# Optimization experiments

Measured on AMD Instinct MI355X. Metric: run time of the kernel, lower is better.

Reference implementation:

```python
import jax, jax.numpy as jnp
import numpy as np

N = 100000
E = 1600000
IN_CH = 32
HID = 64
HEADS = 2
NUM_CLASSES = 12
NEG_SLOPE = 0.2


def gat_conv(x, src, dst, W, a_src, a_dst, bias, concat):
    """PyG-style GATConv (self-loops already appended to src/dst).
    x: [N, F_in], W: [F_in, H*C], a_src/a_dst: [H, C], bias: [H*C] or [C]."""
    n = x.shape[0]
    h = (x @ W).reshape(n, HEADS, -1)                    # [N, H, C]
    al_s = jnp.einsum('nhc,hc->nh', h, a_src)            # [N, H]
    al_d = jnp.einsum('nhc,hc->nh', h, a_dst)            # [N, H]
    e = jax.nn.leaky_relu(al_s[src] + al_d[dst], NEG_SLOPE)  # [Etot, H]
    # segment softmax over destination neighborhoods
    e_max = jax.ops.segment_max(e, dst, num_segments=n)      # [N, H]
    ex = jnp.exp(e - e_max[dst])                              # [Etot, H]
    denom = jax.ops.segment_sum(ex, dst, num_segments=n)     # [N, H]
    alpha = ex / denom[dst]                                   # [Etot, H]
    msg = h[src] * alpha[:, :, None]                          # [Etot, H, C]
    out = jax.ops.segment_sum(msg, dst, num_segments=n)      # [N, H, C]
    if concat:
        out = out.reshape(n, -1)
    else:
        out = out.mean(axis=1)
    return out + bias


def prelu(x, a):
    return jnp.where(x >= 0, x, a * x)


def setup_inputs() -> dict:
    key = jax.random.key(0)
    ks = jax.random.split(key, 16)
    HC = HEADS * HID
    d = {
        'x': jax.random.normal(ks[0], (N, IN_CH), jnp.float32),
        'edge_index': jax.random.randint(ks[1], (2, E), 0, N, jnp.int32),
        'W1': jax.random.normal(ks[2], (IN_CH, HC), jnp.float32) * 0.1,
        'a1s': jax.random.normal(ks[3], (HEADS, HID), jnp.float32) * 0.1,
        'a1d': jax.random.normal(ks[4], (HEADS, HID), jnp.float32) * 0.1,
        'b1': jnp.zeros((HC,), jnp.float32),
        'W2': jax.random.normal(ks[5], (HC, HC), jnp.float32) * 0.1,
        'a2s': jax.random.normal(ks[6], (HEADS, HID), jnp.float32) * 0.1,
        'a2d': jax.random.normal(ks[7], (HEADS, HID), jnp.float32) * 0.1,
        'b2': jnp.zeros((HC,), jnp.float32),
        'W3': jax.random.normal(ks[8], (HC, HC), jnp.float32) * 0.1,
        'a3s': jax.random.normal(ks[9], (HEADS, HID), jnp.float32) * 0.1,
        'a3d': jax.random.normal(ks[10], (HEADS, HID), jnp.float32) * 0.1,
        'b3': jnp.zeros((HID,), jnp.float32),
        'prelu_a': jnp.float32(0.25),
        'Wc': jax.random.normal(ks[11], (HID, NUM_CLASSES), jnp.float32) * 0.1,
        'bc': jnp.zeros((NUM_CLASSES,), jnp.float32),
    }
    return d


def reference(x, edge_index, W1, a1s, a1d, b1, W2, a2s, a2d, b2,
              W3, a3s, a3d, b3, prelu_a, Wc, bc):
    loops = jnp.arange(N, dtype=edge_index.dtype)
    src = jnp.concatenate([edge_index[0], loops])
    dst = jnp.concatenate([edge_index[1], loops])
    h = gat_conv(x, src, dst, W1, a1s, a1d, b1, concat=True)
    h = prelu(h, prelu_a)
    h = gat_conv(h, src, dst, W2, a2s, a2d, b2, concat=True)
    h = prelu(h, prelu_a)
    h = gat_conv(h, src, dst, W3, a3s, a3d, b3, concat=False)
    h = prelu(h, prelu_a)
    return h @ Wc + bc
```

## Files before the change

### kernel.cpp

```cpp
#include <hip/hip_runtime.h>
#include <stdint.h>

#define NN 100000
#define NE 1600000
#define ET (NE + NN)
#define HC 128
#define HID 64
#define NCLS 12
#define BSZ 512
#define NBK ((NN + BSZ - 1) / BSZ)
#define CHUNK 8192
#define NPB ((ET + CHUNK - 1) / CHUNK)

typedef _Float16 f16;
typedef _Float16 f16x2 __attribute__((ext_vector_type(2)));
typedef _Float16 f16x4 __attribute__((ext_vector_type(4)));
typedef _Float16 f16x8 __attribute__((ext_vector_type(8)));
typedef float f32x4 __attribute__((ext_vector_type(4)));

__global__ void k_init(int* bucketTotal) {
    int i = threadIdx.x;
    if (i < NBK) bucketTotal[i] = 0;
}

__global__ __launch_bounds__(256) void k_hist(const int* __restrict__ ei, int* __restrict__ bucketTotal) {
    __shared__ int h[NBK];
    int tid = threadIdx.x;
    for (int b = tid; b < NBK; b += 256) h[b] = 0;
    __syncthreads();
    long base = (long)blockIdx.x * CHUNK;
#pragma unroll
    for (int k = 0; k < CHUNK / 256; k++) {
        long i = base + k * 256 + tid;
        if (i < ET) {
            int d = (i < NE) ? ei[NE + i] : (int)(i - NE);
            atomicAdd(&h[d >> 9], 1);
        }
    }
    __syncthreads();
    for (int b = tid; b < NBK; b += 256)
        if (h[b]) atomicAdd(&bucketTotal[b], h[b]);
}

__global__ __launch_bounds__(256) void k_bscan(const int* __restrict__ bucketTotal,
                                               int* __restrict__ bucketStart,
                                               int* __restrict__ bucketFill,
                                               int* __restrict__ rp) {
    __shared__ int s[256];
    int tid = threadIdx.x;
    int v = (tid < NBK) ? bucketTotal[tid] : 0;
    s[tid] = v;
    __syncthreads();
    for (int o = 1; o < 256; o <<= 1) {
        int t = (tid >= o) ? s[tid - o] : 0;
        __syncthreads();
        s[tid] += t;
        __syncthreads();
    }
    if (tid < NBK) {
        int excl = s[tid] - v;
        bucketStart[tid] = excl;
        bucketFill[tid] = excl;
    }
    if (tid == 0) { bucketStart[NBK] = ET; rp[NN] = ET; }
}

__global__ __launch_bounds__(256) void k_part(const int* __restrict__ ei,
                                              int* __restrict__ bucketFill,
                                              uint32_t* __restrict__ ebuf) {
    __shared__ int h[NBK];
    __shared__ int base[NBK];
    int tid = threadIdx.x;
    for (int b = tid; b < NBK; b += 256) h[b] = 0;
    __syncthreads();
    long cbase = (long)blockIdx.x * CHUNK;
#pragma unroll
    for (int k = 0; k < CHUNK / 256; k++) {
        long i = cbase + k * 256 + tid;
        if (i < ET) {
            int d = (i < NE) ? ei[NE + i] : (int)(i - NE);
            atomicAdd(&h[d >> 9], 1);
        }
    }
    __syncthreads();
    for (int b = tid; b < NBK; b += 256)
        base[b] = h[b] ? atomicAdd(&bucketFill[b], h[b]) : 0;
    __syncthreads();
    for (int b = tid; b < NBK; b += 256) h[b] = 0;
    __syncthreads();
#pragma unroll
    for (int k = 0; k < CHUNK / 256; k++) {
        long i = cbase + k * 256 + tid;
        if (i < ET) {
            int s, d;
            if (i < NE) { s = ei[i]; d = ei[NE + i]; } else { s = d = (int)(i - NE); }
            int bk = d >> 9;
            int off = atomicAdd(&h[bk], 1);
            ebuf[base[bk] + off] = (uint32_t)s | ((uint32_t)(d & 511) << 17);
        }
    }
}

__global__ __launch_bounds__(512) void k_build(const uint32_t* __restrict__ ebuf,
                                               const int* __restrict__ bucketStart,
                                               int* __restrict__ rp, int* __restrict__ colx) {
    __shared__ int cnt[BSZ];
    __shared__ int fill[BSZ];
    int b = blockIdx.x, tid = threadIdx.x;
    int e0 = bucketStart[b], e1 = bucketStart[b + 1], m = e1 - e0;
    cnt[tid] = 0;
    __syncthreads();
    for (int k = tid; k < m; k += 512) atomicAdd(&cnt[ebuf[e0 + k] >> 17], 1);
    __syncthreads();
    int v = cnt[tid];
    __syncthreads();
    cnt[tid] = v;
    __syncthreads();
    for (int o = 1; o < 512; o <<= 1) {
        int t = (tid >= o) ? cnt[tid - o] : 0;
        __syncthreads();
        cnt[tid] += t;
        __syncthreads();
    }
    int excl = cnt[tid] - v;
    int node = b * BSZ + tid;
    if (node < NN) rp[node] = e0 + excl;
    fill[tid] = e0 + excl;
    __syncthreads();
    for (int k = tid; k < m; k += 512) {
        uint32_t e = ebuf[e0 + k];
        int pos = atomicAdd(&fill[e >> 17], 1);
        colx[pos] = (int)(e & 0x1FFFF);
    }
}

__global__ void k_wt(const float* __restrict__ W2, const float* __restrict__ W3,
                     f16* __restrict__ wout) {
    const float* W = blockIdx.x ? W3 : W2;
    f16* hi = wout + (size_t)blockIdx.x * 2 * 2048 * 8;
    f16* lo = hi + 2048 * 8;
    for (int s = threadIdx.x; s < 2048; s += 256) {
        int kk = s >> 9, nt = (s >> 6) & 7, l = s & 63;
        int n = nt * 16 + (l & 15), k0 = kk * 32 + (l >> 4) * 8;
        f16x8 vh, vl;
#pragma unroll
        for (int j = 0; j < 8; j++) {
            float v = W[(long)(k0 + j) * HC + n];
            f16 h = (f16)v;
            vh[j] = h;
            vl[j] = (f16)(v - (float)h);
        }
        *(f16x8*)(hi + (size_t)s * 8) = vh;
        *(f16x8*)(lo + (size_t)s * 8) = vl;
    }
}

__global__ __launch_bounds__(256) void k_att1(const float* __restrict__ x,
                                              const float* __restrict__ W1,
                                              const float* __restrict__ a1s,
                                              const float* __restrict__ a1d,
                                              f16* __restrict__ x16,
                                              float* __restrict__ als, float* __restrict__ ald) {
    __shared__ float sIn[128 * 33];
    __shared__ float spv[128];
    int t = threadIdx.x;
    long n0 = (long)blockIdx.x * 128;
    if (t < 128) {
        int sd = t >> 6, h = (t >> 5) & 1, f = t & 31;
        const float* a = sd ? a1d : a1s;
        float acc = 0.f;
        for (int c = 0; c < 64; c++) acc = fmaf(W1[f * HC + h * 64 + c], a[h * 64 + c], acc);
        spv[t] = acc;
    }
    for (int c = t; c < 128 * 8; c += 256) {
        int row = c >> 3, col = (c & 7) * 4;
        long gn = n0 + row;
        if (gn < NN) {
            float4 v = *(const float4*)(x + gn * 32 + col);
            float* dst = &sIn[row * 33 + col];
            dst[0] = v.x; dst[1] = v.y; dst[2] = v.z; dst[3] = v.w;
            f16x4 o;
            o[0] = (f16)v.x; o[1] = (f16)v.y; o[2] = (f16)v.z; o[3] = (f16)v.w;
            *(f16x4*)(x16 + gn * 32 + col) = o;
        }
    }
    __syncthreads();
    int n = t >> 1, h = t & 1;
    long gn = n0 + n;
    if (gn >= NN) return;
    const float* row = &sIn[n * 33];
    const float* as_ = &spv[h * 32];
    const float* ad_ = &spv[64 + h * 32];
    float s_ = 0.f, d_ = 0.f;
#pragma unroll
    for (int f = 0; f < 32; f++) {
        float v = row[f];
        s_ = fmaf(v, as_[f], s_);
        d_ = fmaf(v, ad_[f], d_);
    }
    als[2 * gn + h] = s_;
    ald[2 * gn + h] = d_;
}

__global__ __launch_bounds__(256) void k_aggx(const int* __restrict__ rp, const int* __restrict__ colx,
                                              const f16* __restrict__ x16,
                                              const float* __restrict__ als, const float* __restrict__ ald,
                                              float* __restrict__ xbar) {
    int wid = blockIdx.x * 4 + (threadIdx.x >> 6);
    int lane = threadIdx.x & 63;
    int g = lane >> 4, li = lane & 15;
    int start = rp[wid], end = rp[wid + 1];
    float2 adv = *(const float2*)(ald + 2 * wid);
    float a00 = 0.f, a01 = 0.f, a10 = 0.f, a11 = 0.f, ws0 = 0.f, ws1 = 0.f;
#pragma unroll 4
    for (int j0 = start; j0 < end; j0 += 4) {
        int j = j0 + g;
        int jc = j < end ? j : end - 1;
        int s = colx[jc];
        float2 asv = *(const float2*)(als + 2 * s);
        float e0 = asv.x + adv.x, e1 = asv.y + adv.y;
        e0 = fmaxf(e0, 0.2f * e0);
        e1 = fmaxf(e1, 0.2f * e1);
        float w0 = __expf(e0), w1 = __expf(e1);
        if (j >= end) { w0 = 0.f; w1 = 0.f; }
        ws0 += w0; ws1 += w1;
        f16x2 xv = *(const f16x2*)(x16 + (long)s * 32 + li * 2);
        float f0 = (float)xv[0], f1 = (float)xv[1];
        a00 = fmaf(w0, f0, a00); a01 = fmaf(w0, f1, a01);
        a10 = fmaf(w1, f0, a10); a11 = fmaf(w1, f1, a11);
    }
#pragma unroll
    for (int o = 16; o <= 32; o <<= 1) {
        ws0 += __shfl_xor(ws0, o); ws1 += __shfl_xor(ws1, o);
        a00 += __shfl_xor(a00, o); a01 += __shfl_xor(a01, o);
        a10 += __shfl_xor(a10, o); a11 += __shfl_xor(a11, o);
    }
    if (g == 0) {
        float inv = 1.0f / ws0;
        *(float2*)(xbar + (long)wid * 64 + li * 2) = make_float2(a00 * inv, a01 * inv);
    } else if (g == 1) {
        float inv = 1.0f / ws1;
        *(float2*)(xbar + (long)wid * 64 + 32 + li * 2) = make_float2(a10 * inv, a11 * inv);
    }
}

__global__ __launch_bounds__(256) void k_post1(const float* __restrict__ xb,
                                               const float* __restrict__ W1,
                                               const float* __restrict__ b1,
                                               const float* __restrict__ pap,
                                               f16* __restrict__ outp) {
    __shared__ __align__(16) float sIn[64 * 64];
    __shared__ __align__(16) float sW[32 * HC];
    __shared__ float sB[HC];
    int tid = threadIdx.x;
    long n0 = (long)blockIdx.x * 64;
    for (int c = tid; c < 64 * 16; c += 256) {
        int row = c >> 4, col = (c & 15) * 4;
        long gn = n0 + row;
        float4 v = make_float4(0.f, 0.f, 0.f, 0.f);
        if (gn < NN) v = *(const float4*)(xb + gn * 64 + col);
        *(float4*)(sIn + row * 64 + col) = v;
    }
    for (int c = tid; c < 32 * HC / 4; c += 256) ((float4*)sW)[c] = ((const float4*)W1)[c];
    if (tid < HC) sB[tid] = b1[tid];
    __syncthreads();
    int cg = tid & 31, ng = tid >> 5, head = cg >> 4;
    float4 acc[8];
#pragma unroll
    for (int i = 0; i < 8; i++) acc[i] = make_float4(0.f, 0.f, 0.f, 0.f);
    for (int k = 0; k < 32; k++) {
        float4 w = *(const float4*)(sW + k * HC + cg * 4);
#pragma unroll
        for (int i = 0; i < 8; i++) {
            float a = sIn[(ng * 8 + i) * 64 + head * 32 + k];
            acc[i].x = fmaf(a, w.x, acc[i].x);
            acc[i].y = fmaf(a, w.y, acc[i].y);
            acc[i].z = fmaf(a, w.z, acc[i].z);
            acc[i].w = fmaf(a, w.w, acc[i].w);
        }
    }
    float pa = pap[0];
    float4 b = *(const float4*)(sB + cg * 4);
#pragma unroll
    for (int i = 0; i < 8; i++) {
        long n = n0 + ng * 8 + i;
        if (n < NN) {
            float o0 = acc[i].x + b.x, o1 = acc[i].y + b.y;
            float o2 = acc[i].z + b.z, o3 = acc[i].w + b.w;
            o0 = o0 >= 0.f ? o0 : pa * o0;
            o1 = o1 >= 0.f ? o1 : pa * o1;
            o2 = o2 >= 0.f ? o2 : pa * o2;
            o3 = o3 >= 0.f ? o3 : pa * o3;
            f16x4 o; o[0] = (f16)o0; o[1] = (f16)o1; o[2] = (f16)o2; o[3] = (f16)o3;
            *(f16x4*)(outp + n * HC + cg * 4) = o;
        }
    }
}

__global__ __launch_bounds__(256) void k_gemmM(const f16* __restrict__ in16,
                                               const f16* __restrict__ wfrag,
                                               const float* __restrict__ avs,
                                               const float* __restrict__ avd,
                                               f16* __restrict__ h16,
                                               float* __restrict__ als, float* __restrict__ ald) {
    const f16* whi = wfrag;
    const f16* wlo = wfrag + 2048 * 8;
    int tid = threadIdx.x;
    int w = tid >> 6, l = tid & 63, q = l >> 4, m = l & 15;
    long n0 = (long)blockIdx.x * 64;
    long rowg = n0 + w * 16 + m;
    bool rok = rowg < NN;
    f32x4 acc[8];
#pragma unroll
    for (int i = 0; i < 8; i++) acc[i] = (f32x4){0.f, 0.f, 0.f, 0.f};
#pragma unroll
    for (int kk = 0; kk < 4; kk++) {
        f16x8 a = {};
        if (rok) a = *(const f16x8*)(in16 + rowg * HC + kk * 32 + q * 8);
#pragma unroll
        for (int nt = 0; nt < 8; nt++) {
            f16x8 bh = *(const f16x8*)(whi + ((kk * 8 + nt) * 64 + l) * 8);
            f16x8 bl = *(const f16x8*)(wlo + ((kk * 8 + nt) * 64 + l) * 8);
            acc[nt] = __builtin_amdgcn_mfma_f32_16x16x32_f16(a, bh, acc[nt], 0, 0, 0);
            acc[nt] = __builtin_amdgcn_mfma_f32_16x16x32_f16(a, bl, acc[nt], 0, 0, 0);
        }
    }
    float as_[8], ad_[8];
#pragma unroll
    for (int nt = 0; nt < 8; nt++) { as_[nt] = avs[nt * 16 + m]; ad_[nt] = avd[nt * 16 + m]; }
#pragma unroll
    for (int r = 0; r < 4; r++) {
        long rg = n0 + w * 16 + q * 4 + r;
        bool ok = rg < NN;
        float s0 = 0.f, s1 = 0.f, d0 = 0.f, d1 = 0.f;
#pragma unroll
        for (int nt = 0; nt < 4; nt++) {
            float v = acc[nt][r];
            s0 = fmaf(v, as_[nt], s0); d0 = fmaf(v, ad_[nt], d0);
        }
#pragma unroll
        for (int nt = 4; nt < 8; nt++) {
            float v = acc[nt][r];
            s1 = fmaf(v, as_[nt], s1); d1 = fmaf(v, ad_[nt], d1);
        }
        if (ok) {
#pragma unroll
            for (int nt = 0; nt < 8; nt++) h16[rg * HC + nt * 16 + m] = (f16)acc[nt][r];
        }
#pragma unroll
        for (int o = 1; o <= 8; o <<= 1) {
            s0 += __shfl_xor(s0, o); s1 += __shfl_xor(s1, o);
            d0 += __shfl_xor(d0, o); d1 += __shfl_xor(d1, o);
        }
        if (ok && m == 0) {
            als[2 * rg] = s0; als[2 * rg + 1] = s1;
            ald[2 * rg] = d0; ald[2 * rg + 1] = d1;
        }
    }
}

template <int MEAN>
__global__ __launch_bounds__(256) void k_agg(const int* __restrict__ rp, const int* __restrict__ colx,
                                             const f16* __restrict__ h,
                                             const float* __restrict__ als, const float* __restrict__ ald,
                                             const float* __restrict__ bias,
                                             const float* __restrict__ pap,
                                             f16* __restrict__ out16,
                                             float* __restrict__ outf) {
    int wid = blockIdx.x * 4 + (threadIdx.x >> 6);
    int lane = threadIdx.x & 63;
    int g = lane >> 4, li = lane & 15;
    int start = rp[wid], end = rp[wid + 1];
    float2 adv = *(const float2*)(ald + 2 * wid);
    float acc[8];
#pragma unroll
    for (int k = 0; k < 8; k++) acc[k] = 0.f;
    float ws0 = 0.f, ws1 = 0.f;
    bool head1 = li >= 8;
#pragma unroll 4
    for (int j0 = start; j0 < end; j0 += 4) {
        int j = j0 + g;
        int jc = j < end ? j : end - 1;
        int s = colx[jc];
        float2 asv = *(const float2*)(als + 2 * s);
        float e0 = asv.x + adv.x, e1 = asv.y + adv.y;
        e0 = fmaxf(e0, 0.2f * e0);
        e1 = fmaxf(e1, 0.2f * e1);
        float w0 = __expf(e0), w1 = __expf(e1);
        if (j >= end) { w0 = 0.f; w1 = 0.f; }
        ws0 += w0; ws1 += w1;
        f16x8 hv = *(const f16x8*)(h + (long)s * HC + li * 8);
        float wsel = head1 ? w1 : w0;
#pragma unroll
        for (int k = 0; k < 8; k++) acc[k] = fmaf(wsel, (float)hv[k], acc[k]);
    }
#pragma unroll
    for (int o = 16; o <= 32; o <<= 1) {
        ws0 += __shfl_xor(ws0, o);
        ws1 += __shfl_xor(ws1, o);
#pragma unroll
        for (int k = 0; k < 8; k++) acc[k] += __shfl_xor(acc[k], o);
    }
    float pa = pap[0];
    if (!MEAN) {
        float inv = 1.0f / (head1 ? ws1 : ws0);
        int c = li * 8 + g * 2;
        float2 bu = *(const float2*)(bias + c);
        float o0 = acc[g * 2] * inv + bu.x;
        float o1 = acc[g * 2 + 1] * inv + bu.y;
        o0 = o0 >= 0.f ? o0 : pa * o0;
        o1 = o1 >= 0.f ? o1 : pa * o1;
        f16x2 o; o[0] = (f16)o0; o[1] = (f16)o1;
        *(f16x2*)(out16 + (long)wid * HC + c) = o;
    } else {
        float inv = 1.0f / (head1 ? ws1 : ws0);
        float v0 = acc[g * 2] * inv, v1 = acc[g * 2 + 1] * inv;
        float p0 = __shfl_xor(v0, 8), p1 = __shfl_xor(v1, 8);
        if (!head1) {
            int c = li * 8 + g * 2;
            float2 bu = *(const float2*)(bias + c);
            float o0 = 0.5f * (v0 + p0) + bu.x;
            float o1 = 0.5f * (v1 + p1) + bu.y;
            o0 = o0 >= 0.f ? o0 : pa * o0;
            o1 = o1 >= 0.f ? o1 : pa * o1;
            *(float2*)(outf + (long)wid * HID + c) = make_float2(o0, o1);
        }
    }
}

__global__ __launch_bounds__(256) void k_cls(const float* __restrict__ hin,
                                             const float* __restrict__ Wc,
                                             const float* __restrict__ bcp,
                                             float* __restrict__ outp) {
    __shared__ float sW[HID * NCLS];
    __shared__ float sb[NCLS];
    int tid = threadIdx.x;
    for (int c = tid; c < HID * NCLS; c += 256) sW[c] = Wc[c];
    if (tid < NCLS) sb[tid] = bcp[tid];
    __syncthreads();
    int n = blockIdx.x * 256 + tid;
    if (n >= NN) return;
    float o[NCLS];
#pragma unroll
    for (int k = 0; k < NCLS; k++) o[k] = sb[k];
    const float* row = hin + (long)n * HID;
#pragma unroll 8
    for (int c = 0; c < HID; c++) {
        float v = row[c];
#pragma unroll
        for (int k = 0; k < NCLS; k++) o[k] = fmaf(v, sW[c * NCLS + k], o[k]);
    }
#pragma unroll
    for (int k = 0; k < NCLS; k += 2)
        *(float2*)(outp + (long)n * NCLS + k) = make_float2(o[k], o[k + 1]);
}

extern "C" void kernel_launch(void* const* d_in, const int* in_sizes, int n_in,
                              void* d_out, int out_size, void* d_ws, size_t ws_size,
                              hipStream_t stream) {
    const float* x   = (const float*)d_in[0];
    const int*   ei  = (const int*)d_in[1];
    const float* W1  = (const float*)d_in[2];
    const float* a1s = (const float*)d_in[3];
    const float* a1d = (const float*)d_in[4];
    const float* b1  = (const float*)d_in[5];
    const float* W2  = (const float*)d_in[6];
    const float* a2s = (const float*)d_in[7];
    const float* a2d = (const float*)d_in[8];
    const float* b2  = (const float*)d_in[9];
    const float* W3  = (const float*)d_in[10];
    const float* a3s = (const float*)d_in[11];
    const float* a3d = (const float*)d_in[12];
    const float* b3  = (const float*)d_in[13];
    const float* pa  = (const float*)d_in[14];
    const float* Wc  = (const float*)d_in[15];
    const float* bc  = (const float*)d_in[16];
    float* out = (float*)d_out;

    char* w = (char*)d_ws;
    size_t off = 0;
    auto take = [&](size_t b) { void* p = w + off; off += (b + 255) & ~(size_t)255; return p; };
    int* rp      = (int*)take((size_t)(NN + 1) * 4);
    int* colx    = (int*)take((size_t)ET * 4);
    int* btot    = (int*)take((size_t)NBK * 4);
    int* bstart  = (int*)take((size_t)(NBK + 1) * 4);
    int* bfill   = (int*)take((size_t)NBK * 4);
    float* als   = (float*)take((size_t)NN * 8);
    float* ald   = (float*)take((size_t)NN * 8);
    f16* wfrag   = (f16*)take((size_t)2 * 2 * 2048 * 8 * 2);
    f16* x16     = (f16*)take((size_t)NN * 32 * 2);
    f16* h16     = (f16*)take((size_t)NN * HC * 2);
    f16* g16     = (f16*)take((size_t)NN * HC * 2);
    float* xbar  = (float*)take((size_t)NN * 64 * 4);
    float* bufB  = (float*)take((size_t)NN * HID * 4);
    uint32_t* ebuf = (uint32_t*)h16;

    int nb = (NN + 255) / 256;
    int gb = (NN + 63) / 64;
    int ab = NN / 4;
    int tb = (NN + 127) / 128;

    k_init<<<1, 256, 0, stream>>>(btot);
    k_hist<<<NPB, 256, 0, stream>>>(ei, btot);
    k_bscan<<<1, 256, 0, stream>>>(btot, bstart, bfill, rp);
    k_part<<<NPB, 256, 0, stream>>>(ei, bfill, ebuf);
    k_build<<<NBK, 512, 0, stream>>>(ebuf, bstart, rp, colx);
    k_wt<<<2, 256, 0, stream>>>(W2, W3, wfrag);

    k_att1<<<tb, 256, 0, stream>>>(x, W1, a1s, a1d, x16, als, ald);
    k_aggx<<<ab, 256, 0, stream>>>(rp, colx, x16, als, ald, xbar);
    k_post1<<<gb, 256, 0, stream>>>(xbar, W1, b1, pa, g16);
    k_gemmM<<<gb, 256, 0, stream>>>(g16, wfrag, a2s, a2d, h16, als, ald);
    k_agg<0><<<ab, 256, 0, stream>>>(rp, colx, h16, als, ald, b2, pa, g16, nullptr);
    k_gemmM<<<gb, 256, 0, stream>>>(g16, wfrag + (size_t)2 * 2048 * 8, a3s, a3d, h16, als, ald);
    k_agg<1><<<ab, 256, 0, stream>>>(rp, colx, h16, als, ald, b3, pa, nullptr, bufB);
    k_cls<<<nb, 256, 0, stream>>>(bufB, Wc, bc, out);
}
```

Baseline: 442.1 us.

## Deterministic per-block histogram partition, fp16 intermediates, LDS-staged GEMM weights, deeper unroll

The edge partitioning now writes per-block bucket histograms to a grid and scans them in one kernel. This drops the init kernel and the second histogram pass in k_part, and removes the global atomics. The xbar and layer-3 output buffers are stored in fp16 instead of fp32 to halve that traffic. k_gemmM stages its hi/lo weight fragments in 64KB of LDS, k_wt is spread over 32 blocks, and the aggregation loops unroll by 8. The risks are extra precision loss from fp16 rounding, lower occupancy in the GEMM from the large LDS use, and a serial column sum over all blocks in k_bscan.

New measurement: 594.9 us. 1.35x slower.

```diff
diff --git a/kernel.cpp b/kernel.cpp
--- a/kernel.cpp
+++ b/kernel.cpp
@@ -18,12 +18,7 @@
 typedef _Float16 f16x8 __attribute__((ext_vector_type(8)));
 typedef float f32x4 __attribute__((ext_vector_type(4)));
 
-__global__ void k_init(int* bucketTotal) {
-    int i = threadIdx.x;
-    if (i < NBK) bucketTotal[i] = 0;
-}
-
-__global__ __launch_bounds__(256) void k_hist(const int* __restrict__ ei, int* __restrict__ bucketTotal) {
+__global__ __launch_bounds__(256) void k_hist(const int* __restrict__ ei, int* __restrict__ hgrid) {
     __shared__ int h[NBK];
     int tid = threadIdx.x;
     for (int b = tid; b < NBK; b += 256) h[b] = 0;
@@ -38,18 +33,18 @@
         }
     }
     __syncthreads();
-    for (int b = tid; b < NBK; b += 256)
-        if (h[b]) atomicAdd(&bucketTotal[b], h[b]);
-}
-
-__global__ __launch_bounds__(256) void k_bscan(const int* __restrict__ bucketTotal,
+    for (int b = tid; b < NBK; b += 256) hgrid[blockIdx.x * NBK + b] = h[b];
+}
+
+__global__ __launch_bounds__(256) void k_bscan(int* __restrict__ hgrid,
                                                int* __restrict__ bucketStart,
-                                               int* __restrict__ bucketFill,
                                                int* __restrict__ rp) {
     __shared__ int s[256];
     int tid = threadIdx.x;
-    int v = (tid < NBK) ? bucketTotal[tid] : 0;
-    s[tid] = v;
+    int tot = 0;
+    if (tid < NBK)
+        for (int b = 0; b < NPB; b++) tot += hgrid[b * NBK + tid];
+    s[tid] = tot;
     __syncthreads();
     for (int o = 1; o < 256; o <<= 1) {
         int t = (tid >= o) ? s[tid - o] : 0;
@@ -57,37 +52,31 @@
         s[tid] += t;
         __syncthreads();
     }
+    int excl = s[tid] - tot;
     if (tid < NBK) {
-        int excl = s[tid] - v;
         bucketStart[tid] = excl;
-        bucketFill[tid] = excl;
+        int run = excl;
+        for (int b = 0; b < NPB; b++) {
+            int t = hgrid[b * NBK + tid];
+            hgrid[b * NBK + tid] = run;
+            run += t;
+        }
     }
     if (tid == 0) { bucketStart[NBK] = ET; rp[NN] = ET; }
 }
 
 __global__ __launch_bounds__(256) void k_part(const int* __restrict__ ei,
-                                              int* __restrict__ bucketFill,
+                                              const int* __restrict__ hgrid,
                                               uint32_t* __restrict__ ebuf) {
     __shared__ int h[NBK];
     __shared__ int base[NBK];
     int tid = threadIdx.x;
-    for (int b = tid; b < NBK; b += 256) h[b] = 0;
+    for (int b = tid; b < NBK; b += 256) {
+        base[b] = hgrid[blockIdx.x * NBK + b];
+        h[b] = 0;
+    }
     __syncthreads();
     long cbase = (long)blockIdx.x * CHUNK;
-#pragma unroll
-    for (int k = 0; k < CHUNK / 256; k++) {
-        long i = cbase + k * 256 + tid;
-        if (i < ET) {
-            int d = (i < NE) ? ei[NE + i] : (int)(i - NE);
-            atomicAdd(&h[d >> 9], 1);
-        }
-    }
-    __syncthreads();
-    for (int b = tid; b < NBK; b += 256)
-        base[b] = h[b] ? atomicAdd(&bucketFill[b], h[b]) : 0;
-    __syncthreads();
-    for (int b = tid; b < NBK; b += 256) h[b] = 0;
-    __syncthreads();
 #pragma unroll
     for (int k = 0; k < CHUNK / 256; k++) {
         long i = cbase + k * 256 + tid;
@@ -136,10 +125,11 @@
 
 __global__ void k_wt(const float* __restrict__ W2, const float* __restrict__ W3,
                      f16* __restrict__ wout) {
-    const float* W = blockIdx.x ? W3 : W2;
-    f16* hi = wout + (size_t)blockIdx.x * 2 * 2048 * 8;
+    int layer = blockIdx.x >> 4, lb = blockIdx.x & 15;
+    const float* W = layer ? W3 : W2;
+    f16* hi = wout + (size_t)layer * 2 * 2048 * 8;
     f16* lo = hi + 2048 * 8;
-    for (int s = threadIdx.x; s < 2048; s += 256) {
+    for (int s = lb * 128 + threadIdx.x; s < (lb + 1) * 128; s += 256) {
         int kk = s >> 9, nt = (s >> 6) & 7, l = s & 63;
         int n = nt * 16 + (l & 15), k0 = kk * 32 + (l >> 4) * 8;
         f16x8 vh, vl;
@@ -205,14 +195,14 @@
 __global__ __launch_bounds__(256) void k_aggx(const int* __restrict__ rp, const int* __restrict__ colx,
                                               const f16* __restrict__ x16,
                                               const float* __restrict__ als, const float* __restrict__ ald,
-                                              float* __restrict__ xbar) {
+                                              f16* __restrict__ xbar) {
     int wid = blockIdx.x * 4 + (threadIdx.x >> 6);
     int lane = threadIdx.x & 63;
     int g = lane >> 4, li = lane & 15;
     int start = rp[wid], end = rp[wid + 1];
     float2 adv = *(const float2*)(ald + 2 * wid);
     float a00 = 0.f, a01 = 0.f, a10 = 0.f, a11 = 0.f, ws0 = 0.f, ws1 = 0.f;
-#pragma unroll 4
+#pragma unroll 8
     for (int j0 = start; j0 < end; j0 += 4) {
         int j = j0 + g;
         int jc = j < end ? j : end - 1;
@@ -237,14 +227,16 @@
     }
     if (g == 0) {
         float inv = 1.0f / ws0;
-        *(float2*)(xbar + (long)wid * 64 + li * 2) = make_float2(a00 * inv, a01 * inv);
+        f16x2 o; o[0] = (f16)(a00 * inv); o[1] = (f16)(a01 * inv);
+        *(f16x2*)(xbar + (long)wid * 64 + li * 2) = o;
     } else if (g == 1) {
         float inv = 1.0f / ws1;
-        *(float2*)(xbar + (long)wid * 64 + 32 + li * 2) = make_float2(a10 * inv, a11 * inv);
-    }
-}
-
-__global__ __launch_bounds__(256) void k_post1(const float* __restrict__ xb,
+        f16x2 o; o[0] = (f16)(a10 * inv); o[1] = (f16)(a11 * inv);
+        *(f16x2*)(xbar + (long)wid * 64 + 32 + li * 2) = o;
+    }
+}
+
+__global__ __launch_bounds__(256) void k_post1(const f16* __restrict__ xb,
                                                const float* __restrict__ W1,
                                                const float* __restrict__ b1,
                                                const float* __restrict__ pap,
@@ -254,12 +246,13 @@
     __shared__ float sB[HC];
     int tid = threadIdx.x;
     long n0 = (long)blockIdx.x * 64;
-    for (int c = tid; c < 64 * 16; c += 256) {
-        int row = c >> 4, col = (c & 15) * 4;
+    for (int c = tid; c < 64 * 8; c += 256) {
+        int row = c >> 3, col = (c & 7) * 8;
         long gn = n0 + row;
-        float4 v = make_float4(0.f, 0.f, 0.f, 0.f);
-        if (gn < NN) v = *(const float4*)(xb + gn * 64 + col);
-        *(float4*)(sIn + row * 64 + col) = v;
+        f16x8 v = {};
+        if (gn < NN) v = *(const f16x8*)(xb + gn * 64 + col);
+#pragma unroll
+        for (int j = 0; j < 8; j++) sIn[row * 64 + col + j] = (float)v[j];
     }
     for (int c = tid; c < 32 * HC / 4; c += 256) ((float4*)sW)[c] = ((const float4*)W1)[c];
     if (tid < HC) sB[tid] = b1[tid];
@@ -303,9 +296,10 @@
                                                const float* __restrict__ avd,
                                                f16* __restrict__ h16,
                                                float* __restrict__ als, float* __restrict__ ald) {
-    const f16* whi = wfrag;
-    const f16* wlo = wfrag + 2048 * 8;
+    extern __shared__ f16 sB[];
     int tid = threadIdx.x;
+    for (int i = tid; i < 4096; i += 256) ((uint4*)sB)[i] = ((const uint4*)wfrag)[i];
+    __syncthreads();
     int w = tid >> 6, l = tid & 63, q = l >> 4, m = l & 15;
     long n0 = (long)blockIdx.x * 64;
     long rowg = n0 + w * 16 + m;
@@ -319,8 +313,8 @@
         if (rok) a = *(const f16x8*)(in16 + rowg * HC + kk * 32 + q * 8);
 #pragma unroll
         for (int nt = 0; nt < 8; nt++) {
-            f16x8 bh = *(const f16x8*)(whi + ((kk * 8 + nt) * 64 + l) * 8);
-            f16x8 bl = *(const f16x8*)(wlo + ((kk * 8 + nt) * 64 + l) * 8);
+            f16x8 bh = *(const f16x8*)(sB + ((kk * 8 + nt) * 64 + l) * 8);
+            f16x8 bl = *(const f16x8*)(sB + 16384 + ((kk * 8 + nt) * 64 + l) * 8);
             acc[nt] = __builtin_amdgcn_mfma_f32_16x16x32_f16(a, bh, acc[nt], 0, 0, 0);
             acc[nt] = __builtin_amdgcn_mfma_f32_16x16x32_f16(a, bl, acc[nt], 0, 0, 0);
         }
@@ -365,8 +359,7 @@
                                              const float* __restrict__ als, const float* __restrict__ ald,
                                              const float* __restrict__ bias,
                                              const float* __restrict__ pap,
-                                             f16* __restrict__ out16,
-                                             float* __restrict__ outf) {
+                                             f16* __restrict__ out16) {
     int wid = blockIdx.x * 4 + (threadIdx.x >> 6);
     int lane = threadIdx.x & 63;
     int g = lane >> 4, li = lane & 15;
@@ -377,7 +370,7 @@
     for (int k = 0; k < 8; k++) acc[k] = 0.f;
     float ws0 = 0.f, ws1 = 0.f;
     bool head1 = li >= 8;
-#pragma unroll 4
+#pragma unroll 8
     for (int j0 = start; j0 < end; j0 += 4) {
         int j = j0 + g;
         int jc = j < end ? j : end - 1;
@@ -423,12 +416,13 @@
             float o1 = 0.5f * (v1 + p1) + bu.y;
             o0 = o0 >= 0.f ? o0 : pa * o0;
             o1 = o1 >= 0.f ? o1 : pa * o1;
-            *(float2*)(outf + (long)wid * HID + c) = make_float2(o0, o1);
-        }
-    }
-}
-
-__global__ __launch_bounds__(256) void k_cls(const float* __restrict__ hin,
+            f16x2 o; o[0] = (f16)o0; o[1] = (f16)o1;
+            *(f16x2*)(out16 + (long)wid * HID + c) = o;
+        }
+    }
+}
+
+__global__ __launch_bounds__(256) void k_cls(const f16* __restrict__ hin,
                                              const float* __restrict__ Wc,
                                              const float* __restrict__ bcp,
                                              float* __restrict__ outp) {
@@ -443,12 +437,17 @@
     float o[NCLS];
 #pragma unroll
     for (int k = 0; k < NCLS; k++) o[k] = sb[k];
-    const float* row = hin + (long)n * HID;
-#pragma unroll 8
-    for (int c = 0; c < HID; c++) {
-        float v = row[c];
-#pragma unroll
-        for (int k = 0; k < NCLS; k++) o[k] = fmaf(v, sW[c * NCLS + k], o[k]);
+    const f16x8* row = (const f16x8*)(hin + (long)n * HID);
+#pragma unroll
+    for (int cc = 0; cc < 8; cc++) {
+        f16x8 rv = row[cc];
+#pragma unroll
+        for (int j = 0; j < 8; j++) {
+            float v = (float)rv[j];
+            int c = cc * 8 + j;
+#pragma unroll
+            for (int k = 0; k < NCLS; k++) o[k] = fmaf(v, sW[c * NCLS + k], o[k]);
+        }
     }
 #pragma unroll
     for (int k = 0; k < NCLS; k += 2)
@@ -482,17 +481,16 @@
     auto take = [&](size_t b) { void* p = w + off; off += (b + 255) & ~(size_t)255; return p; };
     int* rp      = (int*)take((size_t)(NN + 1) * 4);
     int* colx    = (int*)take((size_t)ET * 4);
-    int* btot    = (int*)take((size_t)NBK * 4);
+    int* hgrid   = (int*)take((size_t)NPB * NBK * 4);
     int* bstart  = (int*)take((size_t)(NBK + 1) * 4);
-    int* bfill   = (int*)take((size_t)NBK * 4);
     float* als   = (float*)take((size_t)NN * 8);
     float* ald   = (float*)take((size_t)NN * 8);
     f16* wfrag   = (f16*)take((size_t)2 * 2 * 2048 * 8 * 2);
     f16* x16     = (f16*)take((size_t)NN * 32 * 2);
     f16* h16     = (f16*)take((size_t)NN * HC * 2);
     f16* g16     = (f16*)take((size_t)NN * HC * 2);
-    float* xbar  = (float*)take((size_t)NN * 64 * 4);
-    float* bufB  = (float*)take((size_t)NN * HID * 4);
+    f16* xbar    = (f16*)take((size_t)NN * 64 * 2);
+    f16* mean16  = (f16*)take((size_t)NN * HID * 2);
     uint32_t* ebuf = (uint32_t*)h16;
 
     int nb = (NN + 255) / 256;
@@ -500,19 +498,18 @@
     int ab = NN / 4;
     int tb = (NN + 127) / 128;
 
-    k_init<<<1, 256, 0, stream>>>(btot);
-    k_hist<<<NPB, 256, 0, stream>>>(ei, btot);
-    k_bscan<<<1, 256, 0, stream>>>(btot, bstart, bfill, rp);
-    k_part<<<NPB, 256, 0, stream>>>(ei, bfill, ebuf);
+    k_hist<<<NPB, 256, 0, stream>>>(ei, hgrid);
+    k_bscan<<<1, 256, 0, stream>>>(hgrid, bstart, rp);
+    k_part<<<NPB, 256, 0, stream>>>(ei, hgrid, ebuf);
     k_build<<<NBK, 512, 0, stream>>>(ebuf, bstart, rp, colx);
-    k_wt<<<2, 256, 0, stream>>>(W2, W3, wfrag);
+    k_wt<<<32, 256, 0, stream>>>(W2, W3, wfrag);
 
     k_att1<<<tb, 256, 0, stream>>>(x, W1, a1s, a1d, x16, als, ald);
     k_aggx<<<ab, 256, 0, stream>>>(rp, colx, x16, als, ald, xbar);
     k_post1<<<gb, 256, 0, stream>>>(xbar, W1, b1, pa, g16);
-    k_gemmM<<<gb, 256, 0, stream>>>(g16, wfrag, a2s, a2d, h16, als, ald);
-    k_agg<0><<<ab, 256, 0, stream>>>(rp, colx, h16, als, ald, b2, pa, g16, nullptr);
-    k_gemmM<<<gb, 256, 0, stream>>>(g16, wfrag + (size_t)2 * 2048 * 8, a3s, a3d, h16, als, ald);
-    k_agg<1><<<ab, 256, 0, stream>>>(rp, colx, h16, als, ald, b3, pa, nullptr, bufB);
-    k_cls<<<nb, 256, 0, stream>>>(bufB, Wc, bc, out);
-}
+    k_gemmM<<<gb, 256, 65536, stream>>>(g16, wfrag, a2s, a2d, h16, als, ald);
+    k_agg<0><<<ab, 256, 0, stream>>>(rp, colx, h16, als, ald, b2, pa, g16);
+    k_gemmM<<<gb, 256, 65536, stream>>>(g16, wfrag + (size_t)2 * 2048 * 8, a3s, a3d, h16, als, ald);
+    k_agg<1><<<ab, 256, 0, stream>>>(rp, colx, h16, als, ald, b3, pa, mean16);
+    k_cls<<<nb, 256, 0, stream>>>(mean16, Wc, bc, out);
+}
```
